# Kernel optimization log

Hardware: AMD Instinct MI355X
Metric: run time of the kernel (lower is better)

## Reference

```python
import jax, jax.numpy as jnp
import numpy as np

N, Z_DIM = 131072, 64
K_CODES = 2048
QUANT_TEMP = 0.0  # default T when 'quant_temp' not passed


def setup_inputs() -> dict:
    key = jax.random.key(0)
    k1, k2 = jax.random.split(key)
    z = jax.random.normal(k1, (N, Z_DIM), dtype=jnp.float32)
    e = jax.random.normal(k2, (K_CODES, Z_DIM), dtype=jnp.float32)
    return {"z": z, "e": e}


def reference(z, e):
    # torch.cdist -> euclidean distance matrix [N, K]; argmin over squared
    # distance gives identical indices (sqrt is monotone), so skip the sqrt.
    # ||z - e||^2 = ||z||^2 - 2 z.e^T + ||e||^2
    z_sq = jnp.sum(z * z, axis=1, keepdims=True)          # [N, 1]
    e_sq = jnp.sum(e * e, axis=1)                          # [K]
    d2 = z_sq - 2.0 * (z @ e.T) + e_sq[None, :]            # [N, K]
    min_indices = jnp.argmin(d2, axis=1)                   # [N] int
    z_q = e[min_indices]                                   # gather [N, Z]
    commit_loss = jnp.mean((z - z_q) ** 2)                 # F.mse_loss
    # straight-through: z + (1 - T) * stop_grad(z_q - z), T = 0
    z_out = z + (1.0 - QUANT_TEMP) * jax.lax.stop_gradient(z_q - z)
    return z_out, min_indices, commit_loss
```

## Files before the change

kernel.cpp:

```cpp
#include <hip/hip_runtime.h>


#define N_ROWS 131072
#define ZD 64
#define KCODES 2048
#define RF 4
#define EPS_S 0.02f
#define FLAG_CAP 65536
#define RFIX 4

using f16x8   = __attribute__((ext_vector_type(8))) _Float16;
using floatx4 = __attribute__((ext_vector_type(4))) float;


__global__ __launch_bounds__(256) void prep_kernel(
        const float* __restrict__ e, float* __restrict__ ws) {
    __shared__ float tile[64][65];
    int t = threadIdx.x;
    int c0 = blockIdx.x * 64;
    if (blockIdx.x == 0 && t == 0) { ws[0] = 0.0f; ((unsigned int*)ws)[1] = 0u; }

    float* esn = ws + 1024;
    double* esq64 = (double*)((char*)ws + 16384);
    unsigned short* et = (unsigned short*)((char*)ws + 32768);
    float* eT = (float*)((char*)ws + 557056);

#pragma unroll
    for (int i = 0; i < 16; i++) {
        int idx = i * 256 + t;
        int cc = idx >> 6, k = idx & 63;
        tile[cc][k] = e[(size_t)(c0 + cc) * ZD + k];
    }
    __syncthreads();

    if (t < 64) {
        double s = 0.0;
#pragma unroll
        for (int k = 0; k < 64; k++) { double v = (double)tile[t][k]; s = fma(v, v, s); }
        esq64[c0 + t] = s;
        esn[c0 + t] = (float)(-0.5 * s);
    }

#pragma unroll
    for (int i = 0; i < 16; i++) {
        int idx = i * 256 + t;
        int k = idx >> 6, cc = idx & 63;
        eT[(size_t)k * KCODES + c0 + cc] = tile[cc][k];
    }

#pragma unroll
    for (int i = 0; i < 2; i++) {
        int h = i * 256 + t;
        int tl   = h >> 7;
        int kb   = (h >> 4) & 7;
        int code = h & 15;
        int row  = tl * 16 + code;
        union { _Float16 hf[8]; unsigned int u32[4]; } pk;
#pragma unroll
        for (int j = 0; j < 8; j++) pk.hf[j] = (_Float16)tile[row][kb * 8 + j];
        int gtile = (c0 >> 4) + tl;
        unsigned int* dst = (unsigned int*)(et + (size_t)gtile * 1024 + kb * 128 + code * 8);
        *(uint4*)(void*)dst = *(uint4*)(void*)pk.u32;
    }
}

#define COMPUTE(H0, H1, EN, FCOL) do {                                       \
    floatx4 _ai = {EN, EN, EN, EN};                                          \
    _Pragma("unroll")                                                        \
    for (int _rf = 0; _rf < RF; _rf++) {                                     \
        floatx4 acc;                                                         \
        acc = __builtin_amdgcn_mfma_f32_16x16x32_f16(Fh[_rf][0], H0, _ai, 0, 0, 0); \
        acc = __builtin_amdgcn_mfma_f32_16x16x32_f16(Fh[_rf][1], H1, acc, 0, 0, 0); \
        _Pragma("unroll")                                                    \
        for (int _r = 0; _r < 4; _r++) {                                     \
            float _s  = acc[_r];                                             \
            bool  _gt = _s > mval[_rf][_r];                                  \
            mv2[_rf][_r]  = __builtin_amdgcn_fmed3f(_s, mval[_rf][_r], mv2[_rf][_r]); \
            midx[_rf][_r] = _gt ? (FCOL) : midx[_rf][_r];                    \
            mval[_rf][_r] = fmaxf(_s, mval[_rf][_r]);                        \
        }                                                                    \
    }                                                                        \
} while (0)

#define STAGEP(BUF, P) do {                                                  \
    const char* _src = etiles + ((size_t)((P) & 63) << 12)                   \
                       + ((size_t)threadIdx.x << 4);                         \
    __builtin_amdgcn_global_load_lds(                                        \
        (const __attribute__((address_space(1))) unsigned int*)_src,         \
        (__attribute__((address_space(3))) unsigned int*)&tilebuf[BUF][w << 10], \
        16, 0, 0);                                                           \
} while (0)

#define ITER_R(CT) do {                                                      \
    STAGEP(((CT) + 2) & 3, (CT) + 2);                                        \
    asm volatile("s_waitcnt vmcnt(2)" ::: "memory");                         \
    __builtin_amdgcn_s_barrier();                                            \
    float _en0 = esn_sm[(CT) * 32 + lrow];                                   \
    float _en1 = esn_sm[(CT) * 32 + 16 + lrow];                              \
    const char* _tb = tilebuf[(CT) & 3];                                     \
    f16x8 h0, h1;                                                            \
    h0 = *(const f16x8*)(const void*)(_tb + (lane << 4));                    \
    h1 = *(const f16x8*)(const void*)(_tb + 1024 + (lane << 4));             \
    COMPUTE(h0, h1, _en0, fcol);                                             \
    fcol += 16.0f;                                                           \
    h0 = *(const f16x8*)(const void*)(_tb + 2048 + (lane << 4));             \
    h1 = *(const f16x8*)(const void*)(_tb + 3072 + (lane << 4));             \
    COMPUTE(h0, h1, _en1, fcol);                                             \
    fcol += 16.0f;                                                           \
} while (0)

__global__ __launch_bounds__(256, 2) void vq_mfma(
        const float* __restrict__ z, const float* __restrict__ e,
        float* __restrict__ ws, float* __restrict__ out) {
    const char* etiles = (const char*)ws + 32768;
    unsigned int* cntp  = (unsigned int*)ws + 1;
    unsigned int* flags = (unsigned int*)((char*)ws + 294912);

    __shared__ __attribute__((aligned(16))) char tilebuf[4][4096];
    __shared__ __attribute__((aligned(16))) float esn_sm[KCODES];

    int lane = threadIdx.x & 63;
    int w    = threadIdx.x >> 6;
    int wid  = blockIdx.x * 4 + w;
    int row0 = wid * (RF * 16);
    int lrow = lane & 15;
    int lq   = lane >> 4;

    f16x8 Fh[RF][2];
#pragma unroll
    for (int rf = 0; rf < RF; rf++)
#pragma unroll
        for (int kc = 0; kc < 2; kc++) {
            const float* zp = z + (size_t)(row0 + rf * 16 + lrow) * ZD + kc * 32 + lq * 8;
            float xv[8];
            *(float4*)(void*)&xv[0] = *(const float4*)(const void*)zp;
            *(float4*)(void*)&xv[4] = *(const float4*)(const void*)(zp + 4);
            f16x8 h;
#pragma unroll
            for (int j = 0; j < 8; j++) h[j] = (_Float16)xv[j];
            Fh[rf][kc] = h;
            asm volatile("" : "+v"(Fh[rf][kc]));
        }
    asm volatile("s_waitcnt vmcnt(0)" ::: "memory");

    {
        const char* esrc = (const char*)ws + 4096 + ((size_t)threadIdx.x << 4);
        __builtin_amdgcn_global_load_lds(
            (const __attribute__((address_space(1))) unsigned int*)esrc,
            (__attribute__((address_space(3))) unsigned int*)((char*)esn_sm + (w << 10)),
            16, 0, 0);
        __builtin_amdgcn_global_load_lds(
            (const __attribute__((address_space(1))) unsigned int*)(esrc + 4096),
            (__attribute__((address_space(3))) unsigned int*)((char*)esn_sm + 4096 + (w << 10)),
            16, 0, 0);
    }
    STAGEP(0, 0);
    STAGEP(1, 1);

    floatx4 mval[RF], mv2[RF], midx[RF];
#pragma unroll
    for (int rf = 0; rf < RF; rf++)
#pragma unroll
        for (int r = 0; r < 4; r++) {
            mval[rf][r] = -3.0e38f; mv2[rf][r] = -3.0e38f; midx[rf][r] = 0.0f;
        }

    float fcol = (float)lrow;

    for (int ct = 0; ct < 64; ct += 4) {
        ITER_R(ct);
        ITER_R(ct + 1);
        ITER_R(ct + 2);
        ITER_R(ct + 3);
    }

    float lacc = 0.0f;
#pragma unroll
    for (int rf = 0; rf < RF; rf++)
#pragma unroll
        for (int r = 0; r < 4; r++) {
            float v = mval[rf][r], v2 = mv2[rf][r], fi = midx[rf][r];
            for (int off = 1; off < 16; off <<= 1) {
                float ov  = __shfl_xor(v,  off, 64);
                float ofi = __shfl_xor(fi, off, 64);
                float ov2 = __shfl_xor(v2, off, 64);
                bool take = (ov > v) || ((ov == v) && (ofi < fi));
                float loser = take ? v : ov;
                v2 = fmaxf(fmaxf(v2, ov2), loser);
                v  = take ? ov  : v;
                fi = take ? ofi : fi;
            }
            int row = row0 + rf * 16 + lq * 4 + r;
            int idx = (int)fi;
            float4 ev = ((const float4*)(const void*)(e + (size_t)idx * ZD))[lrow];
            float4 zv = ((const float4*)(const void*)(z + (size_t)row * ZD))[lrow];
            ((float4*)(void*)(out + (size_t)row * ZD))[lrow] = ev;
            float dx = ev.x - zv.x, dy = ev.y - zv.y;
            float dz = ev.z - zv.z, dw = ev.w - zv.w;
            lacc = fmaf(dx, dx, lacc); lacc = fmaf(dy, dy, lacc);
            lacc = fmaf(dz, dz, lacc); lacc = fmaf(dw, dw, lacc);
            if (lrow == 0) {
                out[(size_t)N_ROWS * ZD + row] = fi;
                if (v - v2 < EPS_S) {
                    unsigned int i = atomicAdd(cntp, 1u);
                    if (i < FLAG_CAP) flags[i] = (unsigned int)row;
                }
            }
        }

    for (int off = 1; off < 64; off <<= 1) lacc += __shfl_xor(lacc, off, 64);
    __shared__ float sm[4];
    if (lane == 0) sm[w] = lacc;
    __syncthreads();
    if (threadIdx.x == 0) atomicAdd(ws, sm[0] + sm[1] + sm[2] + sm[3]);
}

__global__ __launch_bounds__(256) void vq_fixup(
        const float* __restrict__ z, const float* __restrict__ e,
        float* __restrict__ ws, float* __restrict__ out) {
    const double* esq64 = (const double*)((const char*)ws + 16384);
    const float* eT = (const float*)((const char*)ws + 557056);
    const unsigned int* flags = (const unsigned int*)((const char*)ws + 294912);
    unsigned int cnt = ((const unsigned int*)ws)[1];
    bool allrows = cnt > FLAG_CAP;
    unsigned int n = allrows ? N_ROWS : cnt;

    if (blockIdx.x == 0 && threadIdx.x == 0)
        out[(size_t)N_ROWS * ZD + N_ROWS] = ws[0] * (1.0f / 8388608.0f);
    if (n == 0) return;

    __shared__ float zrow[RFIX][ZD];
    __shared__ int rows_sm[RFIX];
    __shared__ double sd[4][RFIX]; __shared__ int si[4][RFIX];
    __shared__ int sbest[RFIX];
    int t = threadIdx.x, lane = t & 63, w = t >> 6;

    unsigned int ngroups = (n + RFIX - 1) / RFIX;
    for (unsigned int g = blockIdx.x; g < ngroups; g += gridDim.x) {
        __syncthreads();
        if (t < RFIX) {
            unsigned int u = g * RFIX + (unsigned int)t;
            if (u >= n) u = n - 1;
            rows_sm[t] = allrows ? (int)u : (int)flags[u];
        }
        __syncthreads();
        zrow[t >> 6][t & 63] = z[(size_t)rows_sm[t >> 6] * ZD + (t & 63)];
        __syncthreads();

        double dacc[8][RFIX];
#pragma unroll
        for (int j = 0; j < 8; j++)
#pragma unroll
            for (int r = 0; r < RFIX; r++) dacc[j][r] = 0.0;

        for (int k = 0; k < ZD; k++) {
            const float* ek = eT + k * KCODES + t;
            float e8[8];
#pragma unroll
            for (int j = 0; j < 8; j++) e8[j] = ek[256 * j];
#pragma unroll
            for (int r = 0; r < RFIX; r++) {
                double zk = (double)zrow[r][k];
#pragma unroll
                for (int j = 0; j < 8; j++)
                    dacc[j][r] = fma(zk, (double)e8[j], dacc[j][r]);
            }
        }

#pragma unroll
        for (int r = 0; r < RFIX; r++) {
            double dmin = 1.0e300; int imin = 0;
#pragma unroll
            for (int j = 0; j < 8; j++) {
                int c = t + 256 * j;
                double d = fma(-2.0, dacc[j][r], esq64[c]);
                if (d < dmin) { dmin = d; imin = c; }
            }
            for (int off = 1; off < 64; off <<= 1) {
                double od = __shfl_xor(dmin, off, 64);
                int    oi = __shfl_xor(imin, off, 64);
                if (od < dmin || (od == dmin && oi < imin)) { dmin = od; imin = oi; }
            }
            if (lane == 0) { sd[w][r] = dmin; si[w][r] = imin; }
        }
        __syncthreads();
        if (t < RFIX) {
            double bd = sd[0][t]; int bi = si[0][t];
            for (int q = 1; q < 4; q++)
                if (sd[q][t] < bd || (sd[q][t] == bd && si[q][t] < bi)) {
                    bd = sd[q][t]; bi = si[q][t];
                }
            sbest[t] = bi;
        }
        __syncthreads();
        if (t < 16 * RFIX) {
            int r = t >> 4, pos = t & 15;
            unsigned int u = g * RFIX + (unsigned int)r;
            if (u < n) {
                int row = rows_sm[r]; int bi = sbest[r];
                ((float4*)(void*)(out + (size_t)row * ZD))[pos] =
                    ((const float4*)(const void*)(e + (size_t)bi * ZD))[pos];
                if (pos == 0) out[(size_t)N_ROWS * ZD + row] = (float)bi;
            }
        }
    }
}

extern "C" void kernel_launch(void* const* d_in, const int* in_sizes, int n_in,
                              void* d_out, int out_size, void* d_ws, size_t ws_size,
                              hipStream_t stream) {
    const float* z = (const float*)d_in[0];
    const float* e = (const float*)d_in[1];
    float* out = (float*)d_out;
    float* ws  = (float*)d_ws;

    prep_kernel<<<dim3(32), dim3(256), 0, stream>>>(e, ws);
    vq_mfma<<<dim3(512), dim3(256), 0, stream>>>(z, e, ws, out);
    vq_fixup<<<dim3(1024), dim3(256), 0, stream>>>(z, e, ws, out);
}
```

Before: 180.5 us.

## Add fp32 intermediate fixup tier before fp64 rescoring of ambiguous rows

```diff
diff --git a/kernel.cpp b/kernel.cpp
--- a/kernel.cpp
+++ b/kernel.cpp
@@ -5,8 +5,11 @@
 #define ZD 64
 #define KCODES 2048
 #define RF 4
-#define EPS_S 0.02f
-#define FLAG_CAP 65536
+#define EPS_S 0.014f
+#define FLAG_CAP 49152
+#define FLAG2_CAP 16384
+#define GAP2 1e-3f
+#define RFIX1 8
 #define RFIX 4
 
 using f16x8   = __attribute__((ext_vector_type(8))) _Float16;
@@ -18,7 +21,11 @@
     __shared__ float tile[64][65];
     int t = threadIdx.x;
     int c0 = blockIdx.x * 64;
-    if (blockIdx.x == 0 && t == 0) { ws[0] = 0.0f; ((unsigned int*)ws)[1] = 0u; }
+    if (blockIdx.x == 0 && t == 0) {
+        ws[0] = 0.0f;
+        ((unsigned int*)ws)[1] = 0u;
+        ((unsigned int*)ws)[2] = 0u;
+    }
 
     float* esn = ws + 1024;
     double* esq64 = (double*)((char*)ws + 16384);
@@ -218,15 +225,131 @@
 __global__ __launch_bounds__(256) void vq_fixup(
         const float* __restrict__ z, const float* __restrict__ e,
         float* __restrict__ ws, float* __restrict__ out) {
-    const double* esq64 = (const double*)((const char*)ws + 16384);
+    const float* esn = ws + 1024;
     const float* eT = (const float*)((const char*)ws + 557056);
     const unsigned int* flags = (const unsigned int*)((const char*)ws + 294912);
+    unsigned int* cnt2p = (unsigned int*)ws + 2;
+    unsigned int* flags2 = (unsigned int*)((char*)ws + 491520);
     unsigned int cnt = ((const unsigned int*)ws)[1];
     bool allrows = cnt > FLAG_CAP;
     unsigned int n = allrows ? N_ROWS : cnt;
 
     if (blockIdx.x == 0 && threadIdx.x == 0)
         out[(size_t)N_ROWS * ZD + N_ROWS] = ws[0] * (1.0f / 8388608.0f);
+    if (n == 0) return;
+
+    __shared__ float esn_sm[KCODES];
+    __shared__ float zrow[RFIX1][ZD];
+    __shared__ int rows_sm[RFIX1];
+    __shared__ float sv[4][RFIX1], sv2[4][RFIX1]; __shared__ int si[4][RFIX1];
+    __shared__ int sbest[RFIX1];
+    int t = threadIdx.x, lane = t & 63, w = t >> 6;
+
+#pragma unroll
+    for (int i = 0; i < 8; i++) esn_sm[i * 256 + t] = esn[i * 256 + t];
+
+    unsigned int ngroups = (n + RFIX1 - 1) / RFIX1;
+    for (unsigned int g = blockIdx.x; g < ngroups; g += gridDim.x) {
+        __syncthreads();
+        if (t < RFIX1) {
+            unsigned int u = g * RFIX1 + (unsigned int)t;
+            if (u >= n) u = n - 1;
+            rows_sm[t] = allrows ? (int)u : (int)flags[u];
+            sbest[t] = -1;
+        }
+        __syncthreads();
+        zrow[t >> 6][t & 63]       = z[(size_t)rows_sm[t >> 6] * ZD + (t & 63)];
+        zrow[4 + (t >> 6)][t & 63] = z[(size_t)rows_sm[4 + (t >> 6)] * ZD + (t & 63)];
+        __syncthreads();
+
+        float dacc[8][RFIX1];
+#pragma unroll
+        for (int j = 0; j < 8; j++)
+#pragma unroll
+            for (int r = 0; r < RFIX1; r++) dacc[j][r] = 0.0f;
+
+        for (int k = 0; k < ZD; k++) {
+            const float* ek = eT + k * KCODES + t;
+            float e8[8];
+#pragma unroll
+            for (int j = 0; j < 8; j++) e8[j] = ek[256 * j];
+#pragma unroll
+            for (int r = 0; r < RFIX1; r++) {
+                float zk = zrow[r][k];
+#pragma unroll
+                for (int j = 0; j < 8; j++)
+                    dacc[j][r] = fmaf(zk, e8[j], dacc[j][r]);
+            }
+        }
+
+#pragma unroll
+        for (int r = 0; r < RFIX1; r++) {
+            float v1 = -3.0e38f, v2 = -3.0e38f; int i1 = 0;
+#pragma unroll
+            for (int j = 0; j < 8; j++) {
+                int c = t + 256 * j;
+                float s = dacc[j][r] + esn_sm[c];
+                bool gt = s > v1;
+                v2 = __builtin_amdgcn_fmed3f(s, v1, v2);
+                i1 = gt ? c : i1;
+                v1 = fmaxf(s, v1);
+            }
+            for (int off = 1; off < 64; off <<= 1) {
+                float ov  = __shfl_xor(v1, off, 64);
+                float ov2 = __shfl_xor(v2, off, 64);
+                int   oi  = __shfl_xor(i1, off, 64);
+                bool take = (ov > v1) || ((ov == v1) && (oi < i1));
+                float loser = take ? v1 : ov;
+                v2 = fmaxf(fmaxf(v2, ov2), loser);
+                v1 = take ? ov : v1;
+                i1 = take ? oi : i1;
+            }
+            if (lane == 0) { sv[w][r] = v1; sv2[w][r] = v2; si[w][r] = i1; }
+        }
+        __syncthreads();
+        if (t < RFIX1) {
+            float V = sv[0][t], V2 = sv2[0][t]; int I = si[0][t];
+            for (int q = 1; q < 4; q++) {
+                float ov = sv[q][t], ov2 = sv2[q][t]; int oi = si[q][t];
+                bool take = (ov > V) || ((ov == V) && (oi < I));
+                float loser = take ? V : ov;
+                V2 = fmaxf(fmaxf(V2, ov2), loser);
+                V  = take ? ov : V;
+                I  = take ? oi : I;
+            }
+            unsigned int u = g * RFIX1 + (unsigned int)t;
+            if (u < n) {
+                if (V - V2 < GAP2) {
+                    unsigned int i = atomicAdd(cnt2p, 1u);
+                    if (i < FLAG2_CAP) flags2[i] = (unsigned int)rows_sm[t];
+                } else {
+                    sbest[t] = I;
+                }
+            }
+        }
+        __syncthreads();
+        if (t < 16 * RFIX1) {
+            int r = t >> 4, pos = t & 15;
+            int bi = sbest[r];
+            if (bi >= 0) {
+                int row = rows_sm[r];
+                ((float4*)(void*)(out + (size_t)row * ZD))[pos] =
+                    ((const float4*)(const void*)(e + (size_t)bi * ZD))[pos];
+                if (pos == 0) out[(size_t)N_ROWS * ZD + row] = (float)bi;
+            }
+        }
+    }
+}
+
+__global__ __launch_bounds__(256) void vq_fixup2(
+        const float* __restrict__ z, const float* __restrict__ e,
+        float* __restrict__ ws, float* __restrict__ out) {
+    const double* esq64 = (const double*)((const char*)ws + 16384);
+    const float* eT = (const float*)((const char*)ws + 557056);
+    const unsigned int* flags2 = (const unsigned int*)((const char*)ws + 491520);
+    unsigned int cnt = ((const unsigned int*)ws)[2];
+    bool allrows = cnt > FLAG2_CAP;
+    unsigned int n = allrows ? N_ROWS : cnt;
     if (n == 0) return;
 
     __shared__ float zrow[RFIX][ZD];
@@ -241,7 +364,7 @@
         if (t < RFIX) {
             unsigned int u = g * RFIX + (unsigned int)t;
             if (u >= n) u = n - 1;
-            rows_sm[t] = allrows ? (int)u : (int)flags[u];
+            rows_sm[t] = allrows ? (int)u : (int)flags2[u];
         }
         __syncthreads();
         zrow[t >> 6][t & 63] = z[(size_t)rows_sm[t >> 6] * ZD + (t & 63)];
@@ -317,4 +440,5 @@
     prep_kernel<<<dim3(32), dim3(256), 0, stream>>>(e, ws);
     vq_mfma<<<dim3(512), dim3(256), 0, stream>>>(z, e, ws, out);
     vq_fixup<<<dim3(1024), dim3(256), 0, stream>>>(z, e, ws, out);
+    vq_fixup2<<<dim3(256), dim3(256), 0, stream>>>(z, e, ws, out);
 }
```

New measurement: 207.4 us. +14.9%, slower.
